# Kernel tuning notes

Measured on AMD Instinct MI355X. Metric: run time of the kernel, lower is better.

## Reference

```python
import jax, jax.numpy as jnp
import numpy as np


def setup_inputs() -> dict:
    key = jax.random.key(0)
    k1, k2 = jax.random.split(key)
    B, H, W, D = 4096, 64, 64, 512
    inputs = jax.random.normal(k1, (B, D), dtype=jnp.float32)
    # keras 'random_uniform' initializer default range [-0.05, 0.05]
    weights_map = jax.random.uniform(k2, (H, W, D), dtype=jnp.float32,
                                     minval=-0.05, maxval=0.05)
    return {"inputs": inputs, "weights_map": weights_map}


def reference(inputs, weights_map):
    # inputs: (B, D); weights_map: (H, W, D)
    H, W, D = weights_map.shape
    flat_w = weights_map.reshape(-1, D)              # (N, D), N = H*W
    # avoids materializing the (B, N, D) difference tensor)
    x_sq = jnp.sum(inputs * inputs, axis=1, keepdims=True)    # (B, 1)
    w_sq = jnp.sum(flat_w * flat_w, axis=1)                   # (N,)
    sq_dist = x_sq - 2.0 * (inputs @ flat_w.T) + w_sq         # (B, N)
    sq_dist = jnp.maximum(sq_dist, 0.0)
    bmu_flat = jnp.argmin(sq_dist, axis=1)                    # (B,)
    bmu_y = (bmu_flat // W).astype(jnp.int32)
    bmu_x = (bmu_flat % W).astype(jnp.int32)
    bmu_indices = jnp.stack([bmu_y, bmu_x], axis=1)           # (B, 2)
    min_sq = jnp.take_along_axis(sq_dist, bmu_flat[:, None], axis=1)[:, 0]
    quantization_errors = jnp.sqrt(min_sq)                    # (B,)
    return bmu_indices, quantization_errors
```

## Files before the change

### kernel.cpp

```cpp
#include <hip/hip_runtime.h>

#define B_ROWS 4096
#define N_COLS 4096
#define DIM    512
#define LDK    1024

typedef __attribute__((ext_vector_type(8))) short short8;
typedef __attribute__((ext_vector_type(4))) float floatx4;

__device__ __forceinline__ unsigned short f2bf_rn(float f) {
    unsigned u = __float_as_uint(f);
    u += 0x7fffu + ((u >> 16) & 1u);
    return (unsigned short)(u >> 16);
}
__device__ __forceinline__ float bf2f(unsigned short h) {
    return __uint_as_float(((unsigned)h) << 16);
}

__device__ __forceinline__ unsigned long long pack_key(float v, int idx) {
    unsigned u = __float_as_uint(v);
    u = (u & 0x80000000u) ? ~u : (u | 0x80000000u);
    return ((unsigned long long)u << 32) | (unsigned)idx;
}

__device__ __forceinline__ void async16(const unsigned short* g, unsigned short* l) {
    __builtin_amdgcn_global_load_lds(
        (__attribute__((address_space(1))) void*)g,
        (__attribute__((address_space(3))) void*)l, 16, 0, 0);
}

__global__ __launch_bounds__(256) void som_convert(
    const float* __restrict__ X, const float* __restrict__ Wt,
    unsigned short* __restrict__ Xc, unsigned short* __restrict__ Wc,
    float* __restrict__ x_sq, float* __restrict__ w_sq,
    unsigned long long* __restrict__ packed)
{
    int wave = threadIdx.x >> 6, lane = threadIdx.x & 63;
    int grow = blockIdx.x * 4 + wave;
    bool isX = grow < B_ROWS;
    const float* src = isX ? (X + (size_t)grow * DIM)
                           : (Wt + (size_t)(grow - B_ROWS) * DIM);
    const float4* p4 = (const float4*)src;
    float4 a = p4[lane * 2], b = p4[lane * 2 + 1];
    float f[8] = {a.x, a.y, a.z, a.w, b.x, b.y, b.z, b.w};
    unsigned short hi[8], lo[8];
    float s = 0.f;
    #pragma unroll
    for (int t = 0; t < 8; ++t) {
        hi[t] = f2bf_rn(f[t]);
        lo[t] = f2bf_rn(f[t] - bf2f(hi[t]));
        s = fmaf(f[t], f[t], s);
    }
    unsigned short* dst = (isX ? Xc + (size_t)grow * LDK
                               : Wc + (size_t)(grow - B_ROWS) * LDK) + lane * 8;
    *(ushort4*)(dst)       = make_ushort4(hi[0], hi[1], hi[2], hi[3]);
    *(ushort4*)(dst + 4)   = make_ushort4(hi[4], hi[5], hi[6], hi[7]);
    *(ushort4*)(dst + 512) = make_ushort4(lo[0], lo[1], lo[2], lo[3]);
    *(ushort4*)(dst + 516) = make_ushort4(lo[4], lo[5], lo[6], lo[7]);
    #pragma unroll
    for (int off = 32; off >= 1; off >>= 1) s += __shfl_xor(s, off, 64);
    if (lane == 0) {
        if (isX) { x_sq[grow] = s; packed[grow] = ~0ull; }
        else     { w_sq[grow - B_ROWS] = s; }
    }
}

__global__ __launch_bounds__(512, 2) void som_dist_v2(
    const unsigned short* __restrict__ Xc, const unsigned short* __restrict__ Wc,
    const float* __restrict__ w_sq, unsigned long long* __restrict__ packed)
{
    __shared__ __align__(16) unsigned short L[2 * 64 * 512];
    const int tid  = threadIdx.x;
    const int wave = tid >> 6, lane = tid & 63;
    const int quad = lane >> 4, t16 = lane & 15;
    const int wr = wave >> 2, wc = wave & 3;
    const int bm = blockIdx.y, bn = blockIdx.x;

    const int sg = wave & 3;
    const bool stB = (wave >= 4);
    const unsigned short* gsrc =
        (stB ? Wc + (size_t)bn * 256 * LDK : Xc + (size_t)bm * 256 * LDK)
        + (size_t)(sg * 64 + t16) * LDK + quad * 8;
    unsigned short* const lwav = &L[(stB ? 16384 : 0) + sg * 4096];

    const unsigned short* const pA = &L[wr * 8192 + lane * 8];
    const unsigned short* const pB = &L[16384 + wc * 4096 + lane * 8];

    floatx4 acc[8][4];
    #pragma unroll
    for (int i = 0; i < 8; ++i)
        #pragma unroll
        for (int j = 0; j < 4; ++j) acc[i][j] = (floatx4){0.f, 0.f, 0.f, 0.f};

    #pragma unroll
    for (int q = 0; q < 4; ++q) {
        async16(gsrc + q * 16 * LDK,       lwav + q * 1024);
        async16(gsrc + q * 16 * LDK + 512, lwav + q * 1024 + 512);
    }
    __syncthreads();

    #pragma unroll 2
    for (int kt = 0; kt < 16; ++kt) {
        const int cur = kt & 1;
        const unsigned short* pAc = pA + cur * 32768;
        const unsigned short* pBc = pB + cur * 32768;

        if (kt < 15) {
            const unsigned short* gs = gsrc + (kt + 1) * 32;
            unsigned short* ld = lwav + (cur ^ 1) * 32768;
            #pragma unroll
            for (int q = 0; q < 4; ++q) {
                async16(gs + q * 16 * LDK,       ld + q * 1024);
                async16(gs + q * 16 * LDK + 512, ld + q * 1024 + 512);
            }
        }

        short8 ah[8], bh[4], x4[4];
        #pragma unroll
        for (int i = 0; i < 8; ++i) ah[i] = *(const short8*)(pAc + i * 1024);
        #pragma unroll
        for (int j = 0; j < 4; ++j) bh[j] = *(const short8*)(pBc + j * 1024);
        __builtin_amdgcn_s_setprio(1);
        #pragma unroll
        for (int i = 0; i < 8; ++i)
            #pragma unroll
            for (int j = 0; j < 4; ++j)
                acc[i][j] = __builtin_amdgcn_mfma_f32_16x16x32_bf16(
                    ah[i], bh[j], acc[i][j], 0, 0, 0);
        __builtin_amdgcn_s_setprio(0);

        #pragma unroll
        for (int j = 0; j < 4; ++j) x4[j] = *(const short8*)(pBc + j * 1024 + 512);
        __builtin_amdgcn_s_setprio(1);
        #pragma unroll
        for (int i = 0; i < 8; ++i)
            #pragma unroll
            for (int j = 0; j < 4; ++j)
                acc[i][j] = __builtin_amdgcn_mfma_f32_16x16x32_bf16(
                    ah[i], x4[j], acc[i][j], 0, 0, 0);
        __builtin_amdgcn_s_setprio(0);

        short8 al[8];
        #pragma unroll
        for (int i = 0; i < 8; ++i) al[i] = *(const short8*)(pAc + i * 1024 + 512);
        __builtin_amdgcn_s_setprio(1);
        #pragma unroll
        for (int i = 0; i < 8; ++i)
            #pragma unroll
            for (int j = 0; j < 4; ++j)
                acc[i][j] = __builtin_amdgcn_mfma_f32_16x16x32_bf16(
                    al[i], bh[j], acc[i][j], 0, 0, 0);
        __builtin_amdgcn_s_setprio(0);

        __syncthreads();
    }

    const int col0 = bn * 256 + wc * 64 + t16;
    float wq[4];
    #pragma unroll
    for (int j = 0; j < 4; ++j) wq[j] = w_sq[col0 + j * 16];
    const int row_base = bm * 256 + wr * 128 + quad * 4;
    #pragma unroll
    for (int i = 0; i < 8; ++i) {
        #pragma unroll
        for (int r = 0; r < 4; ++r) {
            unsigned long long best = ~0ull;
            #pragma unroll
            for (int j = 0; j < 4; ++j) {
                float val = fmaf(-2.f, acc[i][j][r], wq[j]);
                unsigned long long key = pack_key(val, col0 + j * 16);
                best = (key < best) ? key : best;
            }
            #pragma unroll
            for (int m = 1; m <= 8; m <<= 1) {
                unsigned long long o = __shfl_xor(best, m, 64);
                best = (o < best) ? o : best;
            }
            if (t16 == 0)
                atomicMin(&packed[row_base + i * 16 + r], best);
        }
    }
}

__global__ __launch_bounds__(256) void som_finalize(
    const unsigned long long* __restrict__ packed,
    const float* __restrict__ x_sq, float* __restrict__ out)
{
    int b = blockIdx.x * 256 + threadIdx.x;
    unsigned long long p = packed[b];
    unsigned idx = (unsigned)(p & 0xffffffffull);
    unsigned key = (unsigned)(p >> 32);
    unsigned u = (key & 0x80000000u) ? (key & 0x7fffffffu) : ~key;
    float val = __uint_as_float(u);
    float sq = fmaxf(x_sq[b] + val, 0.f);
    out[2 * b]     = (float)(idx >> 6);
    out[2 * b + 1] = (float)(idx & 63);
    out[2 * B_ROWS + b] = sqrtf(sq);
}

extern "C" void kernel_launch(void* const* d_in, const int* in_sizes, int n_in,
                              void* d_out, int out_size, void* d_ws, size_t ws_size,
                              hipStream_t stream) {
    const float* X  = (const float*)d_in[0];
    const float* Wt = (const float*)d_in[1];
    float* out = (float*)d_out;

    unsigned long long* packed = (unsigned long long*)d_ws;
    float* x_sq = (float*)((char*)d_ws + (32 << 10));
    float* w_sq = (float*)((char*)d_ws + (48 << 10));
    unsigned short* Xc = (unsigned short*)((char*)d_ws + (64 << 10));
    unsigned short* Wc = (unsigned short*)((char*)d_ws + (64 << 10) + ((size_t)B_ROWS * LDK * 2));

    som_convert<<<dim3((B_ROWS + N_COLS) / 4), dim3(256), 0, stream>>>(
        X, Wt, Xc, Wc, x_sq, w_sq, packed);
    som_dist_v2<<<dim3(N_COLS / 256, B_ROWS / 256), dim3(512), 0, stream>>>(
        Xc, Wc, w_sq, packed);
    som_finalize<<<dim3(B_ROWS / 256), dim3(256), 0, stream>>>(packed, x_sq, out);
}
```

Before: 118.7 us.

## Restructure dist kernel pipeline with explicit vmcnt waits and XCD-aware block swizzle

The GEMM main loop now stages two K-tiles ahead into the double buffer. It uses explicit s_waitcnt vmcnt and raw barriers instead of __syncthreads, and issues the next global-to-LDS copy mid-iteration, once all LDS fragments have been read into registers. All LDS reads are hoisted to the start of each iteration. Block indices are also remapped so that blocks landing on the same XCD share row and column tiles, which should improve L2 reuse. The cost is higher register pressure from holding all fragments at once, plus the correctness risk of hand-tuned waitcnt and barrier placement.

After: 124.1 us. 4.5% more time.

```diff
diff --git a/kernel.cpp b/kernel.cpp
--- a/kernel.cpp
+++ b/kernel.cpp
@@ -65,7 +65,73 @@
     }
 }
 
-__global__ __launch_bounds__(512, 2) void som_dist_v2(
+__device__ __forceinline__ void stage8(const unsigned short* gs, unsigned short* ld) {
+    #pragma unroll
+    for (int q = 0; q < 4; ++q) {
+        async16(gs + q * 16 * LDK,       ld + q * 1024);
+        async16(gs + q * 16 * LDK + 512, ld + q * 1024 + 512);
+    }
+}
+
+__device__ __forceinline__ void dist_iter(
+    int kt, bool do_stage, bool last,
+    const unsigned short* pA, const unsigned short* pB,
+    const unsigned short* gsrc, unsigned short* lwav,
+    floatx4 (&acc)[8][4])
+{
+    const int cur = kt & 1;
+
+    if (last) asm volatile("s_waitcnt vmcnt(0)" ::: "memory");
+    else      asm volatile("s_waitcnt vmcnt(8)" ::: "memory");
+    __builtin_amdgcn_s_barrier();
+    asm volatile("" ::: "memory");
+
+    const unsigned short* pAc = pA + cur * 32768;
+    const unsigned short* pBc = pB + cur * 32768;
+    short8 ah[8], bh[4], bl[4], al[8];
+    #pragma unroll
+    for (int i = 0; i < 8; ++i) ah[i] = *(const short8*)(pAc + i * 1024);
+    #pragma unroll
+    for (int j = 0; j < 4; ++j) bh[j] = *(const short8*)(pBc + j * 1024);
+    #pragma unroll
+    for (int j = 0; j < 4; ++j) bl[j] = *(const short8*)(pBc + j * 1024 + 512);
+    #pragma unroll
+    for (int i = 0; i < 8; ++i) al[i] = *(const short8*)(pAc + i * 1024 + 512);
+
+    __builtin_amdgcn_s_setprio(1);
+    #pragma unroll
+    for (int i = 0; i < 8; ++i)
+        #pragma unroll
+        for (int j = 0; j < 4; ++j)
+            acc[i][j] = __builtin_amdgcn_mfma_f32_16x16x32_bf16(
+                ah[i], bh[j], acc[i][j], 0, 0, 0);
+    __builtin_amdgcn_s_setprio(0);
+
+    __builtin_amdgcn_s_setprio(1);
+    #pragma unroll
+    for (int i = 0; i < 8; ++i)
+        #pragma unroll
+        for (int j = 0; j < 4; ++j)
+            acc[i][j] = __builtin_amdgcn_mfma_f32_16x16x32_bf16(
+                ah[i], bl[j], acc[i][j], 0, 0, 0);
+    __builtin_amdgcn_s_setprio(0);
+
+    asm volatile("s_waitcnt lgkmcnt(0)" ::: "memory");
+    __builtin_amdgcn_s_barrier();
+    asm volatile("" ::: "memory");
+    if (do_stage) stage8(gsrc + (kt + 2) * 32, lwav + cur * 32768);
+
+    __builtin_amdgcn_s_setprio(1);
+    #pragma unroll
+    for (int i = 0; i < 8; ++i)
+        #pragma unroll
+        for (int j = 0; j < 4; ++j)
+            acc[i][j] = __builtin_amdgcn_mfma_f32_16x16x32_bf16(
+                al[i], bh[j], acc[i][j], 0, 0, 0);
+    __builtin_amdgcn_s_setprio(0);
+}
+
+__global__ __launch_bounds__(512, 2) void som_dist_v3(
     const unsigned short* __restrict__ Xc, const unsigned short* __restrict__ Wc,
     const float* __restrict__ w_sq, unsigned long long* __restrict__ packed)
 {
@@ -74,7 +140,11 @@
     const int wave = tid >> 6, lane = tid & 63;
     const int quad = lane >> 4, t16 = lane & 15;
     const int wr = wave >> 2, wc = wave & 3;
-    const int bm = blockIdx.y, bn = blockIdx.x;
+
+    const int bid = blockIdx.y * 16 + blockIdx.x;
+    const int xcd = bid & 7, wix = bid >> 3;
+    const int bm = (xcd >> 2) * 8 + (wix & 7);
+    const int bn = (xcd & 3) * 4 + (wix >> 3);
 
     const int sg = wave & 3;
     const bool stB = (wave >= 4);
@@ -92,68 +162,14 @@
         #pragma unroll
         for (int j = 0; j < 4; ++j) acc[i][j] = (floatx4){0.f, 0.f, 0.f, 0.f};
 
-    #pragma unroll
-    for (int q = 0; q < 4; ++q) {
-        async16(gsrc + q * 16 * LDK,       lwav + q * 1024);
-        async16(gsrc + q * 16 * LDK + 512, lwav + q * 1024 + 512);
-    }
-    __syncthreads();
+    stage8(gsrc,      lwav);
+    stage8(gsrc + 32, lwav + 32768);
 
     #pragma unroll 2
-    for (int kt = 0; kt < 16; ++kt) {
-        const int cur = kt & 1;
-        const unsigned short* pAc = pA + cur * 32768;
-        const unsigned short* pBc = pB + cur * 32768;
-
-        if (kt < 15) {
-            const unsigned short* gs = gsrc + (kt + 1) * 32;
-            unsigned short* ld = lwav + (cur ^ 1) * 32768;
-            #pragma unroll
-            for (int q = 0; q < 4; ++q) {
-                async16(gs + q * 16 * LDK,       ld + q * 1024);
-                async16(gs + q * 16 * LDK + 512, ld + q * 1024 + 512);
-            }
-        }
-
-        short8 ah[8], bh[4], x4[4];
-        #pragma unroll
-        for (int i = 0; i < 8; ++i) ah[i] = *(const short8*)(pAc + i * 1024);
-        #pragma unroll
-        for (int j = 0; j < 4; ++j) bh[j] = *(const short8*)(pBc + j * 1024);
-        __builtin_amdgcn_s_setprio(1);
-        #pragma unroll
-        for (int i = 0; i < 8; ++i)
-            #pragma unroll
-            for (int j = 0; j < 4; ++j)
-                acc[i][j] = __builtin_amdgcn_mfma_f32_16x16x32_bf16(
-                    ah[i], bh[j], acc[i][j], 0, 0, 0);
-        __builtin_amdgcn_s_setprio(0);
-
-        #pragma unroll
-        for (int j = 0; j < 4; ++j) x4[j] = *(const short8*)(pBc + j * 1024 + 512);
-        __builtin_amdgcn_s_setprio(1);
-        #pragma unroll
-        for (int i = 0; i < 8; ++i)
-            #pragma unroll
-            for (int j = 0; j < 4; ++j)
-                acc[i][j] = __builtin_amdgcn_mfma_f32_16x16x32_bf16(
-                    ah[i], x4[j], acc[i][j], 0, 0, 0);
-        __builtin_amdgcn_s_setprio(0);
-
-        short8 al[8];
-        #pragma unroll
-        for (int i = 0; i < 8; ++i) al[i] = *(const short8*)(pAc + i * 1024 + 512);
-        __builtin_amdgcn_s_setprio(1);
-        #pragma unroll
-        for (int i = 0; i < 8; ++i)
-            #pragma unroll
-            for (int j = 0; j < 4; ++j)
-                acc[i][j] = __builtin_amdgcn_mfma_f32_16x16x32_bf16(
-                    al[i], bh[j], acc[i][j], 0, 0, 0);
-        __builtin_amdgcn_s_setprio(0);
-
-        __syncthreads();
-    }
+    for (int kt = 0; kt < 14; ++kt)
+        dist_iter(kt, true, false, pA, pB, gsrc, lwav, acc);
+    dist_iter(14, false, false, pA, pB, gsrc, lwav, acc);
+    dist_iter(15, false, true,  pA, pB, gsrc, lwav, acc);
 
     const int col0 = bn * 256 + wc * 64 + t16;
     float wq[4];
@@ -213,7 +229,7 @@
 
     som_convert<<<dim3((B_ROWS + N_COLS) / 4), dim3(256), 0, stream>>>(
         X, Wt, Xc, Wc, x_sq, w_sq, packed);
-    som_dist_v2<<<dim3(N_COLS / 256, B_ROWS / 256), dim3(512), 0, stream>>>(
+    som_dist_v3<<<dim3(N_COLS / 256, B_ROWS / 256), dim3(512), 0, stream>>>(
         Xc, Wc, w_sq, packed);
     som_finalize<<<dim3(B_ROWS / 256), dim3(256), 0, stream>>>(packed, x_sq, out);
 }
```

## Split GEMM k-step into barrier-synced phases interleaving LDS reads, async loads, MFMA

Applied to the files above, without the earlier changes.

Restructures the main loop of the split-bf16 distance GEMM into six phases. Each phase reads a small set of LDS fragments, issues part of the next tile's async global-to-LDS loads, then runs 16 MFMAs between explicit s_barriers and waitcnts. This spreads memory traffic across the compute and lowers register pressure. It also remaps block IDs so blocks on the same XCD share X/W tiles for better L2 reuse, and vectorizes the convert kernel's stores to 16-byte writes. The extra barriers per k-step add synchronization overhead and rely on manual waitcnt correctness.

New measurement: 124.4 us. +4.8%, slower.

```diff
diff --git a/kernel.cpp b/kernel.cpp
--- a/kernel.cpp
+++ b/kernel.cpp
@@ -43,20 +43,19 @@
     const float4* p4 = (const float4*)src;
     float4 a = p4[lane * 2], b = p4[lane * 2 + 1];
     float f[8] = {a.x, a.y, a.z, a.w, b.x, b.y, b.z, b.w};
-    unsigned short hi[8], lo[8];
+    short8 hi, lo;
     float s = 0.f;
     #pragma unroll
     for (int t = 0; t < 8; ++t) {
-        hi[t] = f2bf_rn(f[t]);
-        lo[t] = f2bf_rn(f[t] - bf2f(hi[t]));
+        unsigned short h = f2bf_rn(f[t]);
+        hi[t] = (short)h;
+        lo[t] = (short)f2bf_rn(f[t] - bf2f(h));
         s = fmaf(f[t], f[t], s);
     }
     unsigned short* dst = (isX ? Xc + (size_t)grow * LDK
                                : Wc + (size_t)(grow - B_ROWS) * LDK) + lane * 8;
-    *(ushort4*)(dst)       = make_ushort4(hi[0], hi[1], hi[2], hi[3]);
-    *(ushort4*)(dst + 4)   = make_ushort4(hi[4], hi[5], hi[6], hi[7]);
-    *(ushort4*)(dst + 512) = make_ushort4(lo[0], lo[1], lo[2], lo[3]);
-    *(ushort4*)(dst + 516) = make_ushort4(lo[4], lo[5], lo[6], lo[7]);
+    *(short8*)(dst)       = hi;
+    *(short8*)(dst + 512) = lo;
     #pragma unroll
     for (int off = 32; off >= 1; off >>= 1) s += __shfl_xor(s, off, 64);
     if (lane == 0) {
@@ -65,7 +64,23 @@
     }
 }
 
-__global__ __launch_bounds__(512, 2) void som_dist_v2(
+#define PH_TAIL(MF)                                            \
+    __builtin_amdgcn_s_barrier();                              \
+    asm volatile("s_waitcnt lgkmcnt(0)");                      \
+    __builtin_amdgcn_s_setprio(1);                             \
+    MF                                                         \
+    __builtin_amdgcn_s_setprio(0);                             \
+    __builtin_amdgcn_s_barrier();
+
+#define MFMA16(AF, BF, I0)                                     \
+    _Pragma("unroll")                                          \
+    for (int i = 0; i < 4; ++i)                                \
+        _Pragma("unroll")                                      \
+        for (int j = 0; j < 4; ++j)                            \
+            acc[(I0) + i][j] = __builtin_amdgcn_mfma_f32_16x16x32_bf16( \
+                AF[i], BF[j], acc[(I0) + i][j], 0, 0, 0);
+
+__global__ __launch_bounds__(512, 2) void som_dist_v4(
     const unsigned short* __restrict__ Xc, const unsigned short* __restrict__ Wc,
     const float* __restrict__ w_sq, unsigned long long* __restrict__ packed)
 {
@@ -74,7 +89,11 @@
     const int wave = tid >> 6, lane = tid & 63;
     const int quad = lane >> 4, t16 = lane & 15;
     const int wr = wave >> 2, wc = wave & 3;
-    const int bm = blockIdx.y, bn = blockIdx.x;
+
+    const int bid = blockIdx.y * 16 + blockIdx.x;
+    const int xcd = bid & 7, wix = bid >> 3;
+    const int bm = (xcd >> 2) * 8 + (wix & 7);
+    const int bn = (xcd & 3) * 4 + (wix >> 3);
 
     const int sg = wave & 3;
     const bool stB = (wave >= 4);
@@ -97,62 +116,63 @@
         async16(gsrc + q * 16 * LDK,       lwav + q * 1024);
         async16(gsrc + q * 16 * LDK + 512, lwav + q * 1024 + 512);
     }
-    __syncthreads();
-
-    #pragma unroll 2
+    asm volatile("s_waitcnt vmcnt(0)");
+    __builtin_amdgcn_s_barrier();
+    __builtin_amdgcn_sched_barrier(0);
+
+    #pragma unroll 1
     for (int kt = 0; kt < 16; ++kt) {
         const int cur = kt & 1;
         const unsigned short* pAc = pA + cur * 32768;
         const unsigned short* pBc = pB + cur * 32768;
-
-        if (kt < 15) {
-            const unsigned short* gs = gsrc + (kt + 1) * 32;
-            unsigned short* ld = lwav + (cur ^ 1) * 32768;
-            #pragma unroll
-            for (int q = 0; q < 4; ++q) {
-                async16(gs + q * 16 * LDK,       ld + q * 1024);
-                async16(gs + q * 16 * LDK + 512, ld + q * 1024 + 512);
-            }
+        const bool st = (kt < 15);
+        const unsigned short* gs = gsrc + (kt + 1) * 32;
+        unsigned short* dst = lwav + (cur ^ 1) * 32768;
+
+        short8 ah0[4], ah1[4], al0[4], al1[4], bh[4], bl[4];
+
+        #pragma unroll
+        for (int i = 0; i < 4; ++i) ah0[i] = *(const short8*)(pAc + i * 1024);
+        #pragma unroll
+        for (int j = 0; j < 4; ++j) bh[j]  = *(const short8*)(pBc + j * 1024);
+        if (st) {
+            async16(gs,                 dst);
+            async16(gs + 512,           dst + 512);
+            async16(gs + 16 * LDK,      dst + 1024);
+            async16(gs + 16 * LDK + 512, dst + 1536);
         }
-
-        short8 ah[8], bh[4], x4[4];
-        #pragma unroll
-        for (int i = 0; i < 8; ++i) ah[i] = *(const short8*)(pAc + i * 1024);
-        #pragma unroll
-        for (int j = 0; j < 4; ++j) bh[j] = *(const short8*)(pBc + j * 1024);
+        PH_TAIL(MFMA16(ah0, bh, 0))
+
+        #pragma unroll
+        for (int j = 0; j < 4; ++j) bl[j] = *(const short8*)(pBc + j * 1024 + 512);
+        if (st) {
+            async16(gs + 32 * LDK,       dst + 2048);
+            async16(gs + 32 * LDK + 512, dst + 2560);
+            async16(gs + 48 * LDK,       dst + 3072);
+            async16(gs + 48 * LDK + 512, dst + 3584);
+        }
+        PH_TAIL(MFMA16(ah0, bl, 0))
+
+        #pragma unroll
+        for (int i = 0; i < 4; ++i) al0[i] = *(const short8*)(pAc + i * 1024 + 512);
+        PH_TAIL(MFMA16(al0, bh, 0))
+
+        #pragma unroll
+        for (int i = 0; i < 4; ++i) ah1[i] = *(const short8*)(pAc + (4 + i) * 1024);
+        PH_TAIL(MFMA16(ah1, bh, 4))
+
+        #pragma unroll
+        for (int i = 0; i < 4; ++i) al1[i] = *(const short8*)(pAc + (4 + i) * 1024 + 512);
+        PH_TAIL(MFMA16(ah1, bl, 4))
+
+        asm volatile("s_waitcnt lgkmcnt(0)");
         __builtin_amdgcn_s_setprio(1);
-        #pragma unroll
-        for (int i = 0; i < 8; ++i)
-            #pragma unroll
-            for (int j = 0; j < 4; ++j)
-                acc[i][j] = __builtin_amdgcn_mfma_f32_16x16x32_bf16(
-                    ah[i], bh[j], acc[i][j], 0, 0, 0);
+        MFMA16(al1, bh, 4)
         __builtin_amdgcn_s_setprio(0);
 
-        #pragma unroll
-        for (int j = 0; j < 4; ++j) x4[j] = *(const short8*)(pBc + j * 1024 + 512);
-        __builtin_amdgcn_s_setprio(1);
-        #pragma unroll
-        for (int i = 0; i < 8; ++i)
-            #pragma unroll
-            for (int j = 0; j < 4; ++j)
-                acc[i][j] = __builtin_amdgcn_mfma_f32_16x16x32_bf16(
-                    ah[i], x4[j], acc[i][j], 0, 0, 0);
-        __builtin_amdgcn_s_setprio(0);
-
-        short8 al[8];
-        #pragma unroll
-        for (int i = 0; i < 8; ++i) al[i] = *(const short8*)(pAc + i * 1024 + 512);
-        __builtin_amdgcn_s_setprio(1);
-        #pragma unroll
-        for (int i = 0; i < 8; ++i)
-            #pragma unroll
-            for (int j = 0; j < 4; ++j)
-                acc[i][j] = __builtin_amdgcn_mfma_f32_16x16x32_bf16(
-                    al[i], bh[j], acc[i][j], 0, 0, 0);
-        __builtin_amdgcn_s_setprio(0);
-
-        __syncthreads();
+        asm volatile("s_waitcnt vmcnt(0)");
+        __builtin_amdgcn_s_barrier();
+        __builtin_amdgcn_sched_barrier(0);
     }
 
     const int col0 = bn * 256 + wc * 64 + t16;
@@ -213,7 +233,7 @@
 
     som_convert<<<dim3((B_ROWS + N_COLS) / 4), dim3(256), 0, stream>>>(
         X, Wt, Xc, Wc, x_sq, w_sq, packed);
-    som_dist_v2<<<dim3(N_COLS / 256, B_ROWS / 256), dim3(512), 0, stream>>>(
+    som_dist_v4<<<dim3(N_COLS / 256, B_ROWS / 256), dim3(512), 0, stream>>>(
         Xc, Wc, w_sq, packed);
     som_finalize<<<dim3(B_ROWS / 256), dim3(256), 0, stream>>>(packed, x_sq, out);
 }
```
